# Performance work log

Hardware: AMD Instinct MI355X
Metric: run time of the kernel (lower is better)

The kernel has to match this reference:

```python
import math
import jax, jax.numpy as jnp
import numpy as np

SCORE_THR = 0.05
NMS_THR = 0.5
MIN_SIZE = 0.01
MAX_DET = 100
SCALE_CLAMP = math.log(1000.0 / 16.0)
WX, WY, WW, WH = 10.0, 10.0, 5.0, 5.0  # BoxCoder weights


def setup_inputs() -> dict:
    key = jax.random.key(0)
    k1, k2, k3, k4 = jax.random.split(key, 4)
    B, N, C = 4, 2048, 3
    H = W = 800
    class_logits = 2.0 * jax.random.normal(k1, (B, N, C), dtype=jnp.float32)
    box_regression = 0.5 * jax.random.normal(k2, (B, N, 4 * C), dtype=jnp.float32)
    cxy = jax.random.uniform(k3, (B, N, 2), minval=0.0, maxval=float(W))
    wh = jax.random.uniform(k4, (B, N, 2), minval=4.0, maxval=100.0)
    proposals = jnp.concatenate([cxy - 0.5 * wh, cxy + 0.5 * wh], axis=-1)
    proposals = jnp.clip(proposals, 0.0, float(W))
    return {"class_logits": class_logits, "box_regression": box_regression,
            "proposals": proposals, "image_h": H, "image_w": W}


def _decode(rel, props):
    # rel: [N, C, 4] deltas, props: [N, 4] xyxy -> [N, C, 4] decoded boxes
    w = props[:, 2] - props[:, 0]
    h = props[:, 3] - props[:, 1]
    cx = props[:, 0] + 0.5 * w
    cy = props[:, 1] + 0.5 * h
    dx = rel[..., 0] / WX
    dy = rel[..., 1] / WY
    dw = jnp.minimum(rel[..., 2] / WW, SCALE_CLAMP)
    dh = jnp.minimum(rel[..., 3] / WH, SCALE_CLAMP)
    pcx = dx * w[:, None] + cx[:, None]
    pcy = dy * h[:, None] + cy[:, None]
    pw = jnp.exp(dw) * w[:, None]
    ph = jnp.exp(dh) * h[:, None]
    return jnp.stack([pcx - 0.5 * pw, pcy - 0.5 * ph,
                      pcx + 0.5 * pw, pcy + 0.5 * ph], axis=-1)


def _pairwise_iou(b):
    # b: [M, 4] -> [M, M]
    area = (b[:, 2] - b[:, 0]) * (b[:, 3] - b[:, 1])
    lt = jnp.maximum(b[:, None, :2], b[None, :, :2])
    rb = jnp.minimum(b[:, None, 2:], b[None, :, 2:])
    whd = jnp.clip(rb - lt, 0.0)
    inter = whd[..., 0] * whd[..., 1]
    return inter / (area[:, None] + area[None, :] - inter + 1e-7)


def _per_image(logits, rel, props, H, W):
    N, C = logits.shape
    scores = jax.nn.softmax(logits, axis=-1)               # [N, C]
    boxes = _decode(rel.reshape(N, C, 4), props)           # [N, C, 4]
    # clip to image (x in [0,W], y in [0,H])
    boxes = jnp.stack([jnp.clip(boxes[..., 0], 0.0, W),
                       jnp.clip(boxes[..., 1], 0.0, H),
                       jnp.clip(boxes[..., 2], 0.0, W),
                       jnp.clip(boxes[..., 3], 0.0, H)], axis=-1)
    # drop background class and flatten -> M = N*(C-1)
    boxes = boxes[:, 1:, :].reshape(-1, 4)
    scores = scores[:, 1:].reshape(-1)
    labels = jnp.broadcast_to(jnp.arange(1, C), (N, C - 1)).reshape(-1)
    valid = ((scores > SCORE_THR)
             & (boxes[:, 2] - boxes[:, 0] >= MIN_SIZE)
             & (boxes[:, 3] - boxes[:, 1] >= MIN_SIZE))
    # batched_nms via per-class coordinate offset
    offset = labels.astype(boxes.dtype) * (jnp.max(boxes) + 1.0)
    ob = boxes + offset[:, None]
    sort_key = jnp.where(valid, scores, -jnp.inf)
    order = jnp.argsort(-sort_key)
    bs, ss, ls, vs, obs = boxes[order], scores[order], labels[order], valid[order], ob[order]
    iou = _pairwise_iou(obs)                               # [M, M]
    M = bs.shape[0]
    idxs = jnp.arange(M)
    def body(i, keep):
        sup = keep[i] & (iou[i] > NMS_THR) & (idxs > i)
        return keep & ~sup
    keep = jax.lax.fori_loop(0, M, body, vs)
    sel = jnp.argsort(~keep, stable=True)[:MAX_DET]        # kept first, score order preserved
    kb, ksc, kl, kk = bs[sel], ss[sel], ls[sel], keep[sel]
    kb = jnp.where(kk[:, None], kb, 0.0)
    ksc = jnp.where(kk, ksc, 0.0)
    kl = jnp.where(kk, kl, 0)
    return kb, ksc, kl, kk


def reference(class_logits, box_regression, proposals, image_h, image_w):
    H = jnp.float32(image_h)
    W = jnp.float32(image_w)
    f = jax.vmap(lambda l, r, p: _per_image(l, r, p, H, W))
    boxes, scores, labels, keep = f(class_logits, box_regression, proposals)
    return boxes, scores, labels, keep
```

## Files before the change

kernel.cpp:

```cpp
#include <hip/hip_runtime.h>
#include <stdint.h>

#define BB 4
#define NN 2048
#define CC 3
#define MM (NN * (CC - 1))
#define MAXDET 100
#define SCORE_THR 0.05f
#define NMS_THR 0.5f
#define MIN_SIZE 0.01f
#define TTARGET 512
#define SSKCAP 1024
#define TILE 128

#define SCORE_OFF (BB * MAXDET * 4)
#define LABEL_OFF (SCORE_OFF + BB * MAXDET)
#define KEEP_OFF (LABEL_OFF + BB * MAXDET)
#define STASH(b, j) (SCORE_OFF + (b) * MAXDET + 96 + (j))

__device__ __forceinline__ void wave_lds_sync() {
  __builtin_amdgcn_wave_barrier();
  __builtin_amdgcn_s_waitcnt(0xC07F);
  __builtin_amdgcn_wave_barrier();
}

__device__ __forceinline__ bool iou_gt(const float4 A, const float aA,
                                       const float4 B, const float aB) {
#pragma clang fp contract(off)
  float ltx = fmaxf(A.x, B.x), lty = fmaxf(A.y, B.y);
  float rbx = fminf(A.z, B.z), rby = fminf(A.w, B.w);
  float iw = fmaxf(rbx - ltx, 0.0f), ih = fmaxf(rby - lty, 0.0f);
  float inter = iw * ih;
  float denom = ((aA + aB) - inter) + 1e-7f;
  return inter / denom > NMS_THR;
}

__global__ __launch_bounds__(512) void decode_kernel(const float* __restrict__ logits,
                                                     const float* __restrict__ rel,
                                                     const float* __restrict__ props,
                                                     const int* __restrict__ ph,
                                                     const int* __restrict__ pw,
                                                     float4* __restrict__ cand_box,
                                                     unsigned long long* __restrict__ keys,
                                                     float* __restrict__ out) {
#pragma clang fp contract(off)
  __shared__ float red[512];
  int tid = threadIdx.x;
  int t = blockIdx.x * 512 + tid;
  int b = t >> 11;
  int n = t & 2047;
  float Hf = (float)ph[0];
  float Wf = (float)pw[0];

  const float* lg = logits + (size_t)t * CC;
  float l0 = lg[0], l1 = lg[1], l2 = lg[2];
  float mx = fmaxf(l0, fmaxf(l1, l2));
  float e0 = expf(l0 - mx), e1 = expf(l1 - mx), e2 = expf(l2 - mx);
  float ssum = (e0 + e1) + e2;

  float4 pr = ((const float4*)props)[t];
  float w = pr.z - pr.x, h = pr.w - pr.y;
  float cx = pr.x + 0.5f * w, cy = pr.y + 0.5f * h;
  const float4* rl = (const float4*)(rel + (size_t)t * 12);
  const float SCALE_CLAMP = 4.135166556742356f;

  float lmax = 0.0f;
  for (int c = 1; c < CC; ++c) {
    float4 rv = rl[c];
    float score = (c == 1 ? e1 : e2) / ssum;
    float dx = rv.x / 10.0f;
    float dy = rv.y / 10.0f;
    float dw = fminf(rv.z / 5.0f, SCALE_CLAMP);
    float dh = fminf(rv.w / 5.0f, SCALE_CLAMP);
    float pcx = dx * w + cx;
    float pcy = dy * h + cy;
    float bw = expf(dw) * w;
    float bh = expf(dh) * h;
    float x1 = pcx - 0.5f * bw, y1 = pcy - 0.5f * bh;
    float x2 = pcx + 0.5f * bw, y2 = pcy + 0.5f * bh;
    x1 = fminf(fmaxf(x1, 0.0f), Wf);
    y1 = fminf(fmaxf(y1, 0.0f), Hf);
    x2 = fminf(fmaxf(x2, 0.0f), Wf);
    y2 = fminf(fmaxf(y2, 0.0f), Hf);

    lmax = fmaxf(lmax, fmaxf(fmaxf(x1, y1), fmaxf(x2, y2)));

    bool valid = (score > SCORE_THR) && (x2 - x1 >= MIN_SIZE) && (y2 - y1 >= MIN_SIZE);
    int m = n * (CC - 1) + (c - 1);
    cand_box[(size_t)b * MM + m] = make_float4(x1, y1, x2, y2);
    unsigned long long key = 0ull;
    if (valid)
      key = (((unsigned long long)__float_as_uint(score)) << 32) |
            (unsigned long long)(0xFFFFFFFFu - (unsigned)m);
    keys[(size_t)b * MM + m] = key;
  }

  red[tid] = lmax;
  __syncthreads();
  for (int s2 = 256; s2 > 0; s2 >>= 1) {
    if (tid < s2) red[tid] = fmaxf(red[tid], red[tid + s2]);
    __syncthreads();
  }
  if (tid == 0) out[STASH(b, blockIdx.x & 3)] = red[0];
}

__device__ void bitonic_sort_desc(unsigned long long* a, int P, int tid) {
  int prev_big = 1;
  for (int size = 2; size <= P; size <<= 1) {
    for (int stride = size >> 1; stride > 0; stride >>= 1) {
      int big = (stride >= 128);
      if (big | prev_big) __syncthreads(); else wave_lds_sync();
      for (int i = tid; i < (P >> 1); i += 512) {
        int lo = 2 * i - (i & (stride - 1));
        int hi = lo + stride;
        bool asc = ((lo & size) != 0);
        unsigned long long x = a[lo], y = a[hi];
        if ((x > y) == asc) { a[lo] = y; a[hi] = x; }
      }
      prev_big = big;
    }
  }
  __syncthreads();
}

__device__ int tiled_nms(const unsigned long long* keys_s, int count,
                         const float4* __restrict__ cbg, float off_base,
                         float4* tob, float4* trb, float* tarea,
                         ulonglong2* smask, int* sflag, int* knew,
                         float4* kept_ob, float4* kept_raw, float* kept_area,
                         unsigned long long* kept_key, int* s_nnew, int tid) {
#pragma clang fp contract(off)
  int wv = tid >> 6, lane = tid & 63;
  int cnt = 0;
  for (int base = 0; base < count && cnt < MAXDET; base += TILE) {
    int tsz = (count - base < TILE) ? (count - base) : TILE;
    if (tid < tsz) {
      unsigned long long key = keys_s[base + tid];
      int m = (int)(0xFFFFFFFFu - (unsigned)key);
      float4 bx = cbg[m];
      int lbl = (m & 1) + 1;
      float off = (float)lbl * off_base;
      float4 ob = make_float4(bx.x + off, bx.y + off, bx.z + off, bx.w + off);
      tob[tid] = ob;
      trb[tid] = bx;
      tarea[tid] = (ob.z - ob.x) * (ob.w - ob.y);
    }
    __syncthreads();

    float4 bi0 = tob[lane];
    float ai0 = tarea[lane];
    float4 bi1 = tob[lane + 64];
    float ai1 = tarea[lane + 64];
    float4 kb0 = kept_ob[(lane < cnt) ? lane : 0];
    float ka0 = kept_area[(lane < cnt) ? lane : 0];
    float4 kb1 = kept_ob[(lane + 64 < cnt) ? lane + 64 : 0];
    float ka1 = kept_area[(lane + 64 < cnt) ? lane + 64 : 0];

    for (int j = wv; j < tsz; j += 8) {
      float4 aj = tob[j];
      float aaj = tarea[j];
      unsigned long long w0 = 0ull, w1 = 0ull;
      if (j < 63) {
        bool p = (lane > j) && (lane < tsz) && iou_gt(aj, aaj, bi0, ai0);
        w0 = __ballot(p);
      }
      if (j < 127) {
        int i = lane + 64;
        bool p = (i > j) && (i < tsz) && iou_gt(aj, aaj, bi1, ai1);
        w1 = __ballot(p);
      }
      bool s = false;
      if (cnt > 0) {
        if (lane < cnt && iou_gt(kb0, ka0, aj, aaj)) s = true;
        if (cnt > 64 && lane + 64 < cnt && iou_gt(kb1, ka1, aj, aaj)) s = true;
      }
      int anyk = __any(s);
      if (lane == 0) {
        smask[j].x = w0;
        smask[j].y = w1;
        sflag[j] = anyk;
      }
    }
    __syncthreads();

    if (tid < 64) {
      int iA = 2 * lane, iB = 2 * lane + 1;
      ulonglong2 rA = smask[(iA < tsz) ? iA : 0];
      ulonglong2 rB = smask[(iB < tsz) ? iB : 0];
      int fA = sflag[(iA < tsz) ? iA : 0];
      int fB = sflag[(iB < tsz) ? iB : 0];
      unsigned long long r0 = 0ull, r1 = 0ull;
      int c = cnt, nk = 0;
      for (int j = 0; j < tsz; ++j) {
        int src = j >> 1;
        unsigned long long m0 = __shfl((j & 1) ? rB.x : rA.x, src);
        unsigned long long m1 = __shfl((j & 1) ? rB.y : rA.y, src);
        int fl = __shfl((j & 1) ? fB : fA, src);
        bool rem = (j < 64) ? ((r0 >> j) & 1ull) : ((r1 >> (j - 64)) & 1ull);
        if (!rem && !fl) {
          if (lane == 0) knew[nk] = j;
          nk++;
          c++;
          r0 |= m0;
          r1 |= m1;
          if (c >= MAXDET) break;
        }
      }
      if (lane == 0) *s_nnew = nk;
    }
    __syncthreads();

    int nnew = *s_nnew;
    if (tid < nnew) {
      int j = knew[tid];
      kept_ob[cnt + tid] = tob[j];
      kept_raw[cnt + tid] = trb[j];
      kept_area[cnt + tid] = tarea[j];
      kept_key[cnt + tid] = keys_s[base + j];
    }
    cnt += nnew;
    __syncthreads();
  }
  return cnt;
}

__global__ __launch_bounds__(512) void nms_kernel(const float4* __restrict__ cand_box,
                                                  const unsigned long long* __restrict__ keys,
                                                  float* __restrict__ out) {
#pragma clang fp contract(off)
  __shared__ __align__(16) unsigned long long sk[MM];
  __shared__ __align__(16) unsigned long long ssk[SSKCAP];
  __shared__ unsigned hist[1024];
  __shared__ __align__(16) float4 tob[TILE];
  __shared__ __align__(16) float4 trb[TILE];
  __shared__ float tarea[TILE];
  __shared__ __align__(16) ulonglong2 smask[TILE];
  __shared__ int sflag[TILE];
  __shared__ int knew[TILE];
  __shared__ float4 kept_ob[MAXDET];
  __shared__ float4 kept_raw[MAXDET];
  __shared__ float kept_area[MAXDET];
  __shared__ unsigned long long kept_key[MAXDET];
  __shared__ int s_scnt, s_thr, s_vtot, s_cnt, s_fb, s_nnew;

  int b = blockIdx.x;
  int tid = threadIdx.x;
  int lane = tid & 63;
  const float4* cbg = cand_box + (size_t)b * MM;

  const ulonglong2* kg = (const ulonglong2*)(keys + (size_t)b * MM);
  ulonglong2 kr[4];
#pragma unroll
  for (int j = 0; j < 4; ++j) kr[j] = kg[j * 512 + tid];

  hist[tid] = 0u;
  hist[tid + 512] = 0u;
  if (tid == 0) { s_scnt = 0; s_thr = 0; s_fb = 0; s_cnt = 0; }
  float m01 = fmaxf(out[STASH(b, 0)], out[STASH(b, 1)]);
  float m23 = fmaxf(out[STASH(b, 2)], out[STASH(b, 3)]);
  float off_base = fmaxf(m01, m23) + 1.0f;
  __syncthreads();

#pragma unroll
  for (int j = 0; j < 4; ++j) {
    unsigned h0 = (unsigned)(kr[j].x >> 32);
    unsigned h1 = (unsigned)(kr[j].y >> 32);
    if (h0) atomicAdd(&hist[(h0 >> 16) & 1023], 1u);
    if (h1) atomicAdd(&hist[(h1 >> 16) & 1023], 1u);
  }
  __syncthreads();

  if (tid < 64) {
    unsigned own[16];
#pragma unroll
    for (int i = 0; i < 16; ++i) own[i] = hist[tid * 16 + i];
    unsigned psum = 0;
#pragma unroll
    for (int i = 0; i < 16; ++i) psum += own[i];
    unsigned s = psum;
    for (int d = 1; d < 64; d <<= 1) {
      unsigned o = __shfl_down(s, d);
      if (tid + d < 64) s += o;
    }
    unsigned after = s - psum;
    int best = -1;
    unsigned run = after;
#pragma unroll
    for (int i = 15; i >= 0; --i) {
      run += own[i];
      if (best < 0 && run >= TTARGET) best = tid * 16 + i;
    }
    int gb = best;
    for (int d = 1; d < 64; d <<= 1) {
      int o = __shfl_down(gb, d);
      if (tid + d < 64) gb = (o > gb) ? o : gb;
    }
    if (tid == 0) {
      s_thr = (gb < 0) ? 0 : gb;
      s_vtot = (int)s;
    }
  }
  __syncthreads();
  int thr = s_thr;
  int Vtot = s_vtot;

#pragma unroll
  for (int j = 0; j < 8; ++j) {
    unsigned long long key = (j & 1) ? kr[j >> 1].y : kr[j >> 1].x;
    unsigned hik = (unsigned)(key >> 32);
    bool pred = (hik != 0u) && ((int)((hik >> 16) & 1023) >= thr);
    unsigned long long mask = __ballot(pred);
    int ofs = __popcll(mask & ((1ull << lane) - 1ull));
    int basea = 0;
    if (lane == 0 && mask) basea = atomicAdd(&s_scnt, (int)__popcll(mask));
    basea = __shfl(basea, 0);
    if (pred) {
      int pos = basea + ofs;
      if (pos < SSKCAP) ssk[pos] = key;
    }
  }
  __syncthreads();
  int T = s_scnt;

  if (T <= SSKCAP) {
    int P = 1;
    while (P < T) P <<= 1;
    for (int i = T + tid; i < P; i += 512) ssk[i] = 0ull;
    __syncthreads();
    bitonic_sort_desc(ssk, P, tid);
    int cnt = tiled_nms(ssk, T, cbg, off_base, tob, trb, tarea, smask, sflag,
                        knew, kept_ob, kept_raw, kept_area, kept_key, &s_nnew, tid);
    if (tid == 0) {
      s_cnt = cnt;
      s_fb = (cnt < MAXDET && T < Vtot) ? 1 : 0;
    }
  } else {
    if (tid == 0) s_fb = 1;
  }
  __syncthreads();

  if (s_fb) {
    ulonglong2* skp = (ulonglong2*)sk;
#pragma unroll
    for (int j = 0; j < 4; ++j) skp[j * 512 + tid] = kr[j];
    __syncthreads();
    bitonic_sort_desc(sk, MM, tid);
    int cnt = tiled_nms(sk, Vtot, cbg, off_base, tob, trb, tarea, smask, sflag,
                        knew, kept_ob, kept_raw, kept_area, kept_key, &s_nnew, tid);
    if (tid == 0) s_cnt = cnt;
    __syncthreads();
  }

  int cnt = s_cnt;
  if (tid < MAXDET) {
    float4 bx = make_float4(0.0f, 0.0f, 0.0f, 0.0f);
    float sc = 0.0f, lb = 0.0f, kp = 0.0f;
    if (tid < cnt) {
      unsigned long long key = kept_key[tid];
      int m = (int)(0xFFFFFFFFu - (unsigned)key);
      bx = kept_raw[tid];
      sc = __uint_as_float((unsigned)(key >> 32));
      lb = (float)((m & 1) + 1);
      kp = 1.0f;
    }
    float* obp = out + (size_t)b * MAXDET * 4 + (size_t)tid * 4;
    obp[0] = bx.x; obp[1] = bx.y; obp[2] = bx.z; obp[3] = bx.w;
    out[SCORE_OFF + b * MAXDET + tid] = sc;
    out[LABEL_OFF + b * MAXDET + tid] = lb;
    out[KEEP_OFF + b * MAXDET + tid] = kp;
  }
}

extern "C" void kernel_launch(void* const* d_in, const int* in_sizes, int n_in,
                              void* d_out, int out_size, void* d_ws, size_t ws_size,
                              hipStream_t stream) {
  const float* logits = (const float*)d_in[0];
  const float* rel = (const float*)d_in[1];
  const float* props = (const float*)d_in[2];
  const int* ph = (const int*)d_in[3];
  const int* pw = (const int*)d_in[4];
  float* out = (float*)d_out;

  char* ws = (char*)d_ws;
  float4* cand_box = (float4*)ws;
  unsigned long long* keys = (unsigned long long*)(ws + (size_t)BB * MM * 16);

  decode_kernel<<<16, 512, 0, stream>>>(logits, rel, props, ph, pw, cand_box, keys, out);
  nms_kernel<<<BB, 512, 0, stream>>>(cand_box, keys, out);
}
```

Measured before the change: 101.0 us.

## Build score histogram in decode, stage survivor boxes in LDS, single-wave sort

The score histogram now comes from global atomics in the decode kernel, so the NMS kernel no longer runs its own LDS histogram pass and two barriers. The candidate target drops to 256, survivor boxes are prefetched into shared memory through a map index, and the small bitonic sort runs on one wave with wave-level syncs only. The cost is an added memset launch, global atomics, and a higher chance of taking the fallback path when the smaller survivor set runs short of detections.

```diff
diff --git a/kernel.cpp b/kernel.cpp
--- a/kernel.cpp
+++ b/kernel.cpp
@@ -9,7 +9,7 @@
 #define SCORE_THR 0.05f
 #define NMS_THR 0.5f
 #define MIN_SIZE 0.01f
-#define TTARGET 512
+#define TTARGET 256
 #define SSKCAP 1024
 #define TILE 128
 
@@ -42,6 +42,7 @@
                                                      const int* __restrict__ pw,
                                                      float4* __restrict__ cand_box,
                                                      unsigned long long* __restrict__ keys,
+                                                     unsigned* __restrict__ hist_g,
                                                      float* __restrict__ out) {
 #pragma clang fp contract(off)
   __shared__ float red[512];
@@ -89,9 +90,12 @@
     int m = n * (CC - 1) + (c - 1);
     cand_box[(size_t)b * MM + m] = make_float4(x1, y1, x2, y2);
     unsigned long long key = 0ull;
-    if (valid)
-      key = (((unsigned long long)__float_as_uint(score)) << 32) |
+    if (valid) {
+      unsigned sb = __float_as_uint(score);
+      key = (((unsigned long long)sb) << 32) |
             (unsigned long long)(0xFFFFFFFFu - (unsigned)m);
+      atomicAdd(&hist_g[b * 1024 + ((sb >> 16) & 1023)], 1u);
+    }
     keys[(size_t)b * MM + m] = key;
   }
 
@@ -102,6 +106,22 @@
     __syncthreads();
   }
   if (tid == 0) out[STASH(b, blockIdx.x & 3)] = red[0];
+}
+
+__device__ void bitonic_sort_desc_wave0(unsigned long long* a, int P, int lane) {
+  for (int size = 2; size <= P; size <<= 1) {
+    for (int stride = size >> 1; stride > 0; stride >>= 1) {
+      wave_lds_sync();
+      for (int i = lane; i < (P >> 1); i += 64) {
+        int lo = 2 * i - (i & (stride - 1));
+        int hi = lo + stride;
+        bool asc = ((lo & size) != 0);
+        unsigned long long x = a[lo], y = a[hi];
+        if ((x > y) == asc) { a[lo] = y; a[hi] = x; }
+      }
+    }
+  }
+  wave_lds_sync();
 }
 
 __device__ void bitonic_sort_desc(unsigned long long* a, int P, int tid) {
@@ -125,6 +145,7 @@
 
 __device__ int tiled_nms(const unsigned long long* keys_s, int count,
                          const float4* __restrict__ cbg, float off_base,
+                         const float4* sboxall, const unsigned short* map, int use_map,
                          float4* tob, float4* trb, float* tarea,
                          ulonglong2* smask, int* sflag, int* knew,
                          float4* kept_ob, float4* kept_raw, float* kept_area,
@@ -137,7 +158,7 @@
     if (tid < tsz) {
       unsigned long long key = keys_s[base + tid];
       int m = (int)(0xFFFFFFFFu - (unsigned)key);
-      float4 bx = cbg[m];
+      float4 bx = use_map ? sboxall[map[m]] : cbg[m];
       int lbl = (m & 1) + 1;
       float off = (float)lbl * off_base;
       float4 ob = make_float4(bx.x + off, bx.y + off, bx.z + off, bx.w + off);
@@ -226,11 +247,13 @@
 
 __global__ __launch_bounds__(512) void nms_kernel(const float4* __restrict__ cand_box,
                                                   const unsigned long long* __restrict__ keys,
+                                                  const unsigned* __restrict__ hist_g,
                                                   float* __restrict__ out) {
 #pragma clang fp contract(off)
   __shared__ __align__(16) unsigned long long sk[MM];
   __shared__ __align__(16) unsigned long long ssk[SSKCAP];
-  __shared__ unsigned hist[1024];
+  __shared__ __align__(16) float4 sbox[SSKCAP];
+  __shared__ unsigned short map[MM];
   __shared__ __align__(16) float4 tob[TILE];
   __shared__ __align__(16) float4 trb[TILE];
   __shared__ float tarea[TILE];
@@ -253,27 +276,16 @@
 #pragma unroll
   for (int j = 0; j < 4; ++j) kr[j] = kg[j * 512 + tid];
 
-  hist[tid] = 0u;
-  hist[tid + 512] = 0u;
-  if (tid == 0) { s_scnt = 0; s_thr = 0; s_fb = 0; s_cnt = 0; }
+  if (tid == 0) { s_scnt = 0; s_fb = 0; s_cnt = 0; }
   float m01 = fmaxf(out[STASH(b, 0)], out[STASH(b, 1)]);
   float m23 = fmaxf(out[STASH(b, 2)], out[STASH(b, 3)]);
   float off_base = fmaxf(m01, m23) + 1.0f;
-  __syncthreads();
-
-#pragma unroll
-  for (int j = 0; j < 4; ++j) {
-    unsigned h0 = (unsigned)(kr[j].x >> 32);
-    unsigned h1 = (unsigned)(kr[j].y >> 32);
-    if (h0) atomicAdd(&hist[(h0 >> 16) & 1023], 1u);
-    if (h1) atomicAdd(&hist[(h1 >> 16) & 1023], 1u);
-  }
-  __syncthreads();
 
   if (tid < 64) {
+    const unsigned* hg = hist_g + b * 1024 + tid * 16;
     unsigned own[16];
 #pragma unroll
-    for (int i = 0; i < 16; ++i) own[i] = hist[tid * 16 + i];
+    for (int i = 0; i < 16; ++i) own[i] = hg[i];
     unsigned psum = 0;
 #pragma unroll
     for (int i = 0; i < 16; ++i) psum += own[i];
@@ -305,18 +317,28 @@
   int Vtot = s_vtot;
 
 #pragma unroll
-  for (int j = 0; j < 8; ++j) {
-    unsigned long long key = (j & 1) ? kr[j >> 1].y : kr[j >> 1].x;
-    unsigned hik = (unsigned)(key >> 32);
-    bool pred = (hik != 0u) && ((int)((hik >> 16) & 1023) >= thr);
-    unsigned long long mask = __ballot(pred);
-    int ofs = __popcll(mask & ((1ull << lane) - 1ull));
-    int basea = 0;
-    if (lane == 0 && mask) basea = atomicAdd(&s_scnt, (int)__popcll(mask));
-    basea = __shfl(basea, 0);
-    if (pred) {
-      int pos = basea + ofs;
-      if (pos < SSKCAP) ssk[pos] = key;
+  for (int j = 0; j < 4; ++j) {
+    int m0 = 1024 * j + 2 * tid;
+    float4 b0 = cbg[m0];
+    float4 b1 = cbg[m0 + 1];
+#pragma unroll
+    for (int half = 0; half < 2; ++half) {
+      unsigned long long key = half ? kr[j].y : kr[j].x;
+      unsigned hik = (unsigned)(key >> 32);
+      bool pred = (hik != 0u) && ((int)((hik >> 16) & 1023) >= thr);
+      unsigned long long mask = __ballot(pred);
+      int ofs = __popcll(mask & ((1ull << lane) - 1ull));
+      int basea = 0;
+      if (lane == 0 && mask) basea = atomicAdd(&s_scnt, (int)__popcll(mask));
+      basea = __shfl(basea, 0);
+      if (pred) {
+        int pos = basea + ofs;
+        if (pos < SSKCAP) {
+          ssk[pos] = key;
+          sbox[pos] = half ? b1 : b0;
+          map[m0 + half] = (unsigned short)pos;
+        }
+      }
     }
   }
   __syncthreads();
@@ -327,9 +349,11 @@
     while (P < T) P <<= 1;
     for (int i = T + tid; i < P; i += 512) ssk[i] = 0ull;
     __syncthreads();
-    bitonic_sort_desc(ssk, P, tid);
-    int cnt = tiled_nms(ssk, T, cbg, off_base, tob, trb, tarea, smask, sflag,
-                        knew, kept_ob, kept_raw, kept_area, kept_key, &s_nnew, tid);
+    if (tid < 64) bitonic_sort_desc_wave0(ssk, P, lane);
+    __syncthreads();
+    int cnt = tiled_nms(ssk, T, cbg, off_base, sbox, map, 1, tob, trb, tarea,
+                        smask, sflag, knew, kept_ob, kept_raw, kept_area,
+                        kept_key, &s_nnew, tid);
     if (tid == 0) {
       s_cnt = cnt;
       s_fb = (cnt < MAXDET && T < Vtot) ? 1 : 0;
@@ -345,8 +369,9 @@
     for (int j = 0; j < 4; ++j) skp[j * 512 + tid] = kr[j];
     __syncthreads();
     bitonic_sort_desc(sk, MM, tid);
-    int cnt = tiled_nms(sk, Vtot, cbg, off_base, tob, trb, tarea, smask, sflag,
-                        knew, kept_ob, kept_raw, kept_area, kept_key, &s_nnew, tid);
+    int cnt = tiled_nms(sk, Vtot, cbg, off_base, sbox, map, 0, tob, trb, tarea,
+                        smask, sflag, knew, kept_ob, kept_raw, kept_area,
+                        kept_key, &s_nnew, tid);
     if (tid == 0) s_cnt = cnt;
     __syncthreads();
   }
@@ -384,7 +409,10 @@
   char* ws = (char*)d_ws;
   float4* cand_box = (float4*)ws;
   unsigned long long* keys = (unsigned long long*)(ws + (size_t)BB * MM * 16);
-
-  decode_kernel<<<16, 512, 0, stream>>>(logits, rel, props, ph, pw, cand_box, keys, out);
-  nms_kernel<<<BB, 512, 0, stream>>>(cand_box, keys, out);
-}
+  unsigned* hist_g = (unsigned*)(ws + (size_t)BB * MM * 16 + (size_t)BB * MM * 8);
+
+  hipMemsetAsync(hist_g, 0, BB * 1024 * sizeof(unsigned), stream);
+  decode_kernel<<<16, 512, 0, stream>>>(logits, rel, props, ph, pw, cand_box,
+                                        keys, hist_g, out);
+  nms_kernel<<<BB, 512, 0, stream>>>(cand_box, keys, hist_g, out);
+}
```

Result: slower. 111.5 us (+10.5%).
